# Kernel optimization log

Hardware: AMD Instinct MI355X
Metric: run time of the kernel (lower is better)

Reference implementation:

```python
import jax, jax.numpy as jnp
from jax import lax
import numpy as np

KEY = 4
WIDTH = 32
CH = 3


def _inv_perm():
    # Reproduce construct_mapping(4, 32, 3): mapping[0] = arange(384),
    # mapping[1] = blocks of a (4,32,3) index grid split into 4x4x3 column
    # blocks, flattened. tensor_map does out[:, perm] = in[:, arange], i.e.
    # a scatter; equivalently out = in[:, argsort(perm)].
    s = np.arange(KEY * WIDTH * CH).reshape(KEY, WIDTH, CH)
    perm = np.concatenate([s[:, j:j + KEY, :].reshape(-1) for j in range(0, WIDTH, KEY)])
    return np.argsort(perm)  # (384,)

_INV = jnp.asarray(_inv_perm())


def _conv(x, w, b):
    y = lax.conv_general_dilated(x, w, (1, 1), 'SAME',
                                 dimension_numbers=('NCHW', 'OIHW', 'NCHW'))
    return y + b[None, :, None, None]


def _maxpool2(x):
    return lax.reduce_window(x, -jnp.inf, lax.max,
                             (1, 1, 2, 2), (1, 1, 2, 2), 'VALID')


def setup_inputs() -> dict:
    key = jax.random.key(0)
    ks = jax.random.split(key, 10)
    f32 = jnp.float32
    B = 8192
    return {
        'x': jax.random.normal(ks[0], (B, 32, 32, 3), dtype=f32),
        'W_lin': jax.random.normal(ks[1], (48, 48), dtype=f32) * 0.1,
        'conv1_w': jax.random.normal(ks[2], (32, 3, 3, 3), dtype=f32) * 0.1,
        'conv1_b': jax.random.normal(ks[3], (32,), dtype=f32) * 0.05,
        'conv2_w': jax.random.normal(ks[4], (64, 32, 3, 3), dtype=f32) * 0.05,
        'conv2_b': jax.random.normal(ks[5], (64,), dtype=f32) * 0.05,
        'conv3_w': jax.random.normal(ks[6], (128, 64, 3, 3), dtype=f32) * 0.05,
        'conv3_b': jax.random.normal(ks[7], (128,), dtype=f32) * 0.05,
        'fc_w': jax.random.normal(ks[8], (10, 2048), dtype=f32) * 0.02,
        'fc_b': jax.random.normal(ks[9], (10,), dtype=f32) * 0.02,
        'stage': 2,
    }


def reference(x, W_lin, conv1_w, conv1_b, conv2_w, conv2_b, conv3_w, conv3_b,
              fc_w, fc_b, stage):
    B = x.shape[0]
    if stage == 2:
        # 64 blocks of 4x4x3 in row-major block order (i outer, j inner).
        xb = x.reshape(B, 8, KEY, 8, KEY, CH)            # (B, ib, ir, jb, jc, c)
        xb = xb.transpose(0, 1, 3, 2, 4, 5).reshape(B, 64, 48)
        y = jnp.einsum('bnk,ok->bno', xb, W_lin)          # per-block linear (no bias)
        # group 8 column-blocks per row-block -> (B, 8, 384), permute columns
        y = y.reshape(B, 8, 384)[:, :, _INV]
        x_final = y.reshape(B, 32, 32, 3).transpose(0, 3, 1, 2)  # NCHW
    else:
        x_final = x
    h = _maxpool2(jax.nn.relu(_conv(x_final, conv1_w, conv1_b)))
    h = _maxpool2(jax.nn.relu(_conv(h, conv2_w, conv2_b)))
    h = _maxpool2(jax.nn.relu(_conv(h, conv3_w, conv3_b)))
    h = h.reshape(-1, 2048)
    logits = h @ fc_w.T + fc_b
    return jax.nn.log_softmax(logits, axis=-1)
```

## Files before the change

kernel.cpp:

```cpp
#include <hip/hip_runtime.h>
#include <hip/hip_bf16.h>

typedef unsigned short u16;
typedef __attribute__((ext_vector_type(8))) short short8v;
typedef __attribute__((ext_vector_type(4))) float f32x4;
typedef __attribute__((ext_vector_type(16))) float f32x16;
typedef union { short8v v; uint u[4]; } pack8;

__device__ __forceinline__ float bu2f(u16 u) {
    return __uint_as_float(((unsigned)u) << 16);
}
__device__ __forceinline__ u16 f2bu(float f) {
    unsigned u = __float_as_uint(f);
    u += 0x7fffu + ((u >> 16) & 1u);
    return (u16)(u >> 16);
}
__device__ __forceinline__ uint pk2(float a, float b) {
    return (uint)f2bu(a) | ((uint)f2bu(b) << 16);
}

__global__ __launch_bounds__(256) void k_repack(
    const float* __restrict__ Wlin, const float* __restrict__ c1w,
    const float* __restrict__ c2w, const float* __restrict__ c3w,
    u16* __restrict__ w1p, u16* __restrict__ s2wp,
    u16* __restrict__ w2p, u16* __restrict__ w3p)
{
    int i = blockIdx.x * 256 + threadIdx.x;
    if (i < 32 * 48) {
        int oc = i / 48, k = i - oc * 48;
        int kh = k >> 4, e = k & 15;
        int kw = e >> 2, c = e & 3;
        u16 v = 0;
        if (kw < 3 && c < 3)
            v = f2bu(c1w[((oc * 3 + c) * 3 + kh) * 3 + kw]);
        w1p[i] = v;
    }
    if (i < 96 * 72) {
        int r = i / 72, k = i - r * 72;
        u16 v = 0;
        if (k < 48) {
            int o = r % 48;
            float w = Wlin[o * 48 + k];
            u16 hi = f2bu(w);
            v = (r < 48) ? hi : f2bu(w - bu2f(hi));
        }
        s2wp[i] = v;
    }
    if (i < 64 * 288) {
        int oc = i / 288, r = i - oc * 288;
        int tap = r >> 5, ic = r & 31;
        w2p[oc * 296 + r] = f2bu(c2w[(oc * 32 + ic) * 9 + tap]);
    }
    if (i < 128 * 576) {
        int oc = i / 576, r = i - oc * 576;
        int tap = r >> 6, ic = r & 63;
        w3p[oc * 584 + r] = f2bu(c3w[(oc * 64 + ic) * 9 + tap]);
    }
}

#define IMG4  0
#define SCR   4624
#define IN3   4624
#define W1L   11024
#define IN2   12560
#define LDS_N 25520

__global__ __launch_bounds__(256, 3) void k_img(
    const float* __restrict__ x, const u16* __restrict__ s2wp,
    const u16* __restrict__ w1p, const float* __restrict__ c1b,
    const int* __restrict__ stage,
    const u16* __restrict__ w2p, const float* __restrict__ c2b,
    const u16* __restrict__ w3p, const float* __restrict__ c3b,
    u16* __restrict__ o3)
{
    __shared__ __align__(16) u16 lds[LDS_N];
    const int b = blockIdx.x, t = threadIdx.x;
    const int wv = t >> 6, lane = t & 63, lr = lane & 15, q = lane >> 4;
    uint* z32 = (uint*)lds;

    for (int i = t; i < 2312; i += 256) z32[i] = 0u;
    for (int i = t; i < 1360; i += 256) {
        int cell = i / 20, d = i - cell * 20;
        int h, w;
        if (cell < 18)      { h = 0;  w = cell; }
        else if (cell < 36) { h = 17; w = cell - 18; }
        else { int k = cell - 36; h = 1 + (k >> 1); w = (k & 1) * 17; }
        z32[6280 + (h * 18 + w) * 20 + d] = 0u;
    }
    for (int i = t; i < 192; i += 256)
        *(short8v*)(&lds[W1L + i * 8]) = *(const short8v*)(&w1p[i * 8]);

    const int sv = stage[0];
    if (sv == 2) {
        {
            const int n = t >> 2, ir = t & 3;
            const float* xp = x + (size_t)b * 3072 + (((n >> 3) * 4 + ir) * 96 + (n & 7) * 12);
            const float4 va = ((const float4*)xp)[0];
            const float4 vb = ((const float4*)xp)[1];
            const float4 vc = ((const float4*)xp)[2];
            uint* dst = (uint*)&lds[SCR + n * 72 + ir * 12];
            dst[0] = pk2(va.x, va.y); dst[1] = pk2(va.z, va.w);
            dst[2] = pk2(vb.x, vb.y); dst[3] = pk2(vb.z, vb.w);
            dst[4] = pk2(vc.x, vc.y); dst[5] = pk2(vc.z, vc.w);
            if (ir < 2) {
                uint* z2 = (uint*)&lds[SCR + n * 72 + 48 + ir * 8];
                z2[0] = 0u; z2[1] = 0u; z2[2] = 0u; z2[3] = 0u;
            }
        }
        short8v bh0[3], bh1[3], bl0[3], bl1[3];
        #pragma unroll
        for (int nf = 0; nf < 3; ++nf) {
            bh0[nf] = *(const short8v*)(&s2wp[(nf * 16 + lr) * 72 + q * 8]);
            bh1[nf] = *(const short8v*)(&s2wp[(nf * 16 + lr) * 72 + 32 + q * 8]);
            bl0[nf] = *(const short8v*)(&s2wp[(48 + nf * 16 + lr) * 72 + q * 8]);
            bl1[nf] = *(const short8v*)(&s2wp[(48 + nf * 16 + lr) * 72 + 32 + q * 8]);
        }
        __syncthreads();
        short8v a0 = *(const short8v*)&lds[SCR + (wv * 16 + lr) * 72 + q * 8];
        short8v a1 = *(const short8v*)&lds[SCR + (wv * 16 + lr) * 72 + 32 + q * 8];
        f32x4 y[3];
        #pragma unroll
        for (int nf = 0; nf < 3; ++nf) {
            y[nf] = (f32x4){0.f, 0.f, 0.f, 0.f};
            y[nf] = __builtin_amdgcn_mfma_f32_16x16x32_bf16(a0, bh0[nf], y[nf], 0, 0, 0);
            y[nf] = __builtin_amdgcn_mfma_f32_16x16x32_bf16(a1, bh1[nf], y[nf], 0, 0, 0);
            y[nf] = __builtin_amdgcn_mfma_f32_16x16x32_bf16(a0, bl0[nf], y[nf], 0, 0, 0);
            y[nf] = __builtin_amdgcn_mfma_f32_16x16x32_bf16(a1, bl1[nf], y[nf], 0, 0, 0);
        }
        #pragma unroll
        for (int nf = 0; nf < 3; ++nf)
            #pragma unroll
            for (int r = 0; r < 4; ++r) {
                int n2 = wv * 16 + q * 4 + r;
                int o  = nf * 16 + lr;
                int ir = o / 12, rm = o - ir * 12;
                int jc = rm / 3, c = rm - jc * 3;
                int hh = (n2 >> 3) * 4 + ir, ww = (n2 & 7) * 4 + jc;
                lds[IMG4 + ((hh + 1) * 34 + (ww + 1)) * 4 + c] = f2bu(y[nf][r]);
            }
    } else {
        if (t < 4) z32[2312 + t] = 0u;
        __syncthreads();
        for (int e = t; e < 3072; e += 256) {
            int hh = e / 96, rm = e - hh * 96;
            int ww = rm / 3, c = rm - ww * 3;
            lds[IMG4 + ((hh + 1) * 34 + (ww + 1)) * 4 + c] = f2bu(x[(size_t)b * 3072 + e]);
        }
    }
    __syncthreads();

    for (int i = t; i < 1152; i += 256) {
        int cell = i >> 5, d = i & 31;
        int pos;
        if (cell < 10)      pos = cell;
        else if (cell < 20) pos = 90 + (cell - 10);
        else { int k = cell - 20; pos = (1 + (k >> 1)) * 10 + (k & 1) * 9; }
        z32[2312 + pos * 32 + d] = 0u;
    }
    {
        const int oc32 = lane & 31, hi = lane >> 5;
        short8v wb[3];
        #pragma unroll
        for (int s = 0; s < 3; ++s)
            wb[s] = *(const short8v*)&lds[W1L + oc32 * 48 + s * 16 + hi * 8];
        const float bias1 = c1b[oc32];

        #pragma unroll
        for (int chk = 0; chk < 4; ++chk) {
            f32x16 acc0, acc1;
            #pragma unroll
            for (int i = 0; i < 16; ++i) { acc0[i] = 0.f; acc1[i] = 0.f; }
            #pragma unroll
            for (int s = 0; s < 3; ++s) {
                #pragma unroll
                for (int f = 0; f < 2; ++f) {
                    const int h = wv * 8 + chk * 2 + f;
                    const int a4 = ((h + s) * 34 + oc32 + hi * 2) * 4;
                    pack8 pk;
                    *(unsigned long long*)&pk.u[0] = *(const unsigned long long*)(&lds[IMG4 + a4]);
                    *(unsigned long long*)&pk.u[2] = *(const unsigned long long*)(&lds[IMG4 + a4 + 4]);
                    if (f == 0) acc0 = __builtin_amdgcn_mfma_f32_32x32x16_bf16(pk.v, wb[s], acc0, 0, 0, 0);
                    else        acc1 = __builtin_amdgcn_mfma_f32_32x32x16_bf16(pk.v, wb[s], acc1, 0, 0, 0);
                }
            }
            const int hq = wv * 4 + chk;
            #pragma unroll
            for (int g = 0; g < 4; ++g) {
                #pragma unroll
                for (int pp = 0; pp < 2; ++pp) {
                    const int i0 = 4 * g + 2 * pp;
                    float m0 = fmaxf(acc0[i0], acc0[i0 + 1]);
                    float m1 = fmaxf(acc1[i0], acc1[i0 + 1]);
                    float v = fmaxf(fmaxf(m0, m1) + bias1, 0.f);
                    const int wq = 4 * g + 2 * hi + pp;
                    lds[IN2 + ((hq + 1) * 18 + (wq + 1)) * 40 + oc32] = f2bu(v);
                }
            }
        }
    }
    __syncthreads();

    {
        const u16* wb2 = w2p + (size_t)lr * 296 + q * 8;
        f32x4 acc[4][4];
        #pragma unroll
        for (int m = 0; m < 4; ++m)
            #pragma unroll
            for (int n = 0; n < 4; ++n) acc[m][n] = (f32x4){0.f, 0.f, 0.f, 0.f};

        short8v bfr[3][4];
        #pragma unroll
        for (int n = 0; n < 4; ++n) {
            bfr[0][n] = *(const short8v*)(wb2 + n * 4736 + 0);
            bfr[1][n] = *(const short8v*)(wb2 + n * 4736 + 32);
        }
        #pragma unroll
        for (int s = 0; s < 9; ++s) {
            if (s + 2 < 9) {
                #pragma unroll
                for (int n = 0; n < 4; ++n)
                    bfr[(s + 2) % 3][n] = *(const short8v*)(wb2 + n * 4736 + (s + 2) * 32);
            }
            const int kh = s / 3, kw = s - kh * 3;
            short8v af[4];
            #pragma unroll
            for (int m = 0; m < 4; ++m)
                af[m] = *(const short8v*)(&lds[IN2 + ((wv * 4 + m + kh) * 18 + lr + kw) * 40 + q * 8]);
            __builtin_amdgcn_s_setprio(1);
            #pragma unroll
            for (int m = 0; m < 4; ++m)
                #pragma unroll
                for (int n = 0; n < 4; ++n)
                    acc[m][n] = __builtin_amdgcn_mfma_f32_16x16x32_bf16(af[m], bfr[s % 3][n], acc[m][n], 0, 0, 0);
            __builtin_amdgcn_s_setprio(0);
        }
        #pragma unroll
        for (int n = 0; n < 4; ++n) {
            float bias = c2b[n * 16 + lr];
            #pragma unroll
            for (int mp = 0; mp < 2; ++mp) {
                #pragma unroll
                for (int p = 0; p < 2; ++p) {
                    float m0 = fmaxf(acc[2 * mp][n][2 * p], acc[2 * mp][n][2 * p + 1]);
                    float m1 = fmaxf(acc[2 * mp + 1][n][2 * p], acc[2 * mp + 1][n][2 * p + 1]);
                    float v = fmaxf(fmaxf(m0, m1) + bias, 0.f);
                    int hq = wv * 2 + mp, wq = 2 * q + p;
                    int posW = (hq + 1) * 10 + (wq + 1);
                    int oc = n * 16 + lr;
                    lds[IN3 + posW * 64 + (oc ^ ((posW & 7) << 3))] = f2bu(v);
                }
            }
        }
    }
    __syncthreads();

    {
        const int ocb = wv * 32;
        const int hA = lr >> 3, wA = lr & 7;
        const u16* wb3 = w3p + (size_t)(ocb + lr) * 584 + q * 8;

        f32x4 acc3[4][2];
        #pragma unroll
        for (int m = 0; m < 4; ++m)
            #pragma unroll
            for (int n = 0; n < 2; ++n) acc3[m][n] = (f32x4){0.f, 0.f, 0.f, 0.f};

        short8v br[3][2];
        #pragma unroll
        for (int n = 0; n < 2; ++n) {
            br[0][n] = *(const short8v*)(wb3 + n * 9344 + 0);
            br[1][n] = *(const short8v*)(wb3 + n * 9344 + 32);
        }
        #pragma unroll
        for (int s = 0; s < 18; ++s) {
            if (s + 2 < 18) {
                const int off2 = ((s + 2) >> 1) * 64 + ((s + 2) & 1) * 32;
                #pragma unroll
                for (int n = 0; n < 2; ++n)
                    br[(s + 2) % 3][n] = *(const short8v*)(wb3 + n * 9344 + off2);
            }
            const int tap = s >> 1, half = s & 1;
            const int kh = tap / 3, kw = tap - kh * 3;
            short8v a3[4];
            #pragma unroll
            for (int m = 0; m < 4; ++m) {
                int posR = (m * 2 + hA + kh) * 10 + wA + kw;
                int sl = (half * 32 + q * 8) ^ ((posR & 7) << 3);
                a3[m] = *(const short8v*)(&lds[IN3 + posR * 64 + sl]);
            }
            __builtin_amdgcn_s_setprio(1);
            #pragma unroll
            for (int m = 0; m < 4; ++m)
                #pragma unroll
                for (int n = 0; n < 2; ++n)
                    acc3[m][n] = __builtin_amdgcn_mfma_f32_16x16x32_bf16(a3[m], br[s % 3][n], acc3[m][n], 0, 0, 0);
            __builtin_amdgcn_s_setprio(0);
        }
        #pragma unroll
        for (int n = 0; n < 2; ++n) {
            float bias = c3b[ocb + n * 16 + lr];
            #pragma unroll
            for (int m = 0; m < 4; ++m) {
                #pragma unroll
                for (int p = 0; p < 2; ++p) {
                    float mm = fmaxf(acc3[m][n][2 * p], acc3[m][n][2 * p + 1]);
                    float v2 = fmaxf(mm, __shfl_xor(mm, 32));
                    float v = fmaxf(v2 + bias, 0.f);
                    if (lane < 32) {
                        int wq = (q & 1) * 2 + p;
                        o3[(size_t)b * 2048 + (m * 4 + wq) * 128 + ocb + n * 16 + lr] = f2bu(v);
                    }
                }
            }
        }
    }
}

__global__ __launch_bounds__(256) void k_fc(
    const u16* __restrict__ o3, const float* __restrict__ fw,
    const float* __restrict__ fb, float* __restrict__ out)
{
    const int b = blockIdx.x * 4 + (threadIdx.x >> 6);
    const int lane = threadIdx.x & 63;
    const u16* xp = o3 + (size_t)b * 2048;
    float xr[32];
    #pragma unroll
    for (int i = 0; i < 32; ++i) {
        int kk = lane + i * 64;
        int c = kk >> 4, h = (kk >> 2) & 3, w = kk & 3;
        xr[i] = bu2f(xp[h * 512 + w * 128 + c]);
    }
    float lg[10];
    #pragma unroll
    for (int o = 0; o < 10; ++o) {
        const float* wr = fw + (size_t)o * 2048;
        float s = 0.f;
        #pragma unroll
        for (int i = 0; i < 32; ++i) s += xr[i] * wr[lane + i * 64];
        #pragma unroll
        for (int d = 32; d > 0; d >>= 1) s += __shfl_xor(s, d);
        lg[o] = s + fb[o];
    }
    float m = lg[0];
    #pragma unroll
    for (int o = 1; o < 10; ++o) m = fmaxf(m, lg[o]);
    float den = 0.f;
    #pragma unroll
    for (int o = 0; o < 10; ++o) den += expf(lg[o] - m);
    float lse = logf(den);
    if (lane < 10) {
        float v = lg[0];
        #pragma unroll
        for (int o = 1; o < 10; ++o) v = (lane == o) ? lg[o] : v;
        out[(size_t)b * 10 + lane] = v - m - lse;
    }
}

extern "C" void kernel_launch(void* const* d_in, const int* in_sizes, int n_in,
                              void* d_out, int out_size, void* d_ws, size_t ws_size,
                              hipStream_t stream)
{
    const float* x    = (const float*)d_in[0];
    const float* Wlin = (const float*)d_in[1];
    const float* c1w  = (const float*)d_in[2];
    const float* c1b  = (const float*)d_in[3];
    const float* c2w  = (const float*)d_in[4];
    const float* c2b  = (const float*)d_in[5];
    const float* c3w  = (const float*)d_in[6];
    const float* c3b  = (const float*)d_in[7];
    const float* fw   = (const float*)d_in[8];
    const float* fb   = (const float*)d_in[9];
    const int* stage  = (const int*)d_in[10];
    float* out = (float*)d_out;

    const int B = in_sizes[0] / 3072;

    char* ws = (char*)d_ws;
    u16* o3   = (u16*)ws;
    char* WB  = ws + (size_t)B * 4096;
    u16* w1p  = (u16*)(WB);
    u16* s2wp = (u16*)(WB + 4608);
    u16* w2p  = (u16*)(WB + 18432);
    u16* w3p  = (u16*)(WB + 56320);

    k_repack<<<288, 256, 0, stream>>>(Wlin, c1w, c2w, c3w, w1p, s2wp, w2p, w3p);
    k_img   <<<B, 256, 0, stream>>>(x, s2wp, w1p, c1b, stage, w2p, c2b, w3p, c3b, o3);
    k_fc    <<<B / 4, 256, 0, stream>>>(o3, fw, fb, out);
}
```

Before: 258.4 us.

## Shrink LDS footprint and split conv2 accumulators to raise occupancy to 4 blocks

```diff
diff --git a/kernel.cpp b/kernel.cpp
--- a/kernel.cpp
+++ b/kernel.cpp
@@ -59,13 +59,12 @@
 }
 
 #define IMG4  0
-#define SCR   4624
-#define IN3   4624
-#define W1L   11024
-#define IN2   12560
-#define LDS_N 25520
-
-__global__ __launch_bounds__(256, 3) void k_img(
+#define XB    4624
+#define IN3   0
+#define IN2   6400
+#define LDS_N 19360
+
+__global__ __launch_bounds__(256, 4) void k_img(
     const float* __restrict__ x, const u16* __restrict__ s2wp,
     const u16* __restrict__ w1p, const float* __restrict__ c1b,
     const int* __restrict__ stage,
@@ -76,19 +75,14 @@
     __shared__ __align__(16) u16 lds[LDS_N];
     const int b = blockIdx.x, t = threadIdx.x;
     const int wv = t >> 6, lane = t & 63, lr = lane & 15, q = lane >> 4;
+    const int oc32 = lane & 31, hi = lane >> 5;
     uint* z32 = (uint*)lds;
 
     for (int i = t; i < 2312; i += 256) z32[i] = 0u;
-    for (int i = t; i < 1360; i += 256) {
-        int cell = i / 20, d = i - cell * 20;
-        int h, w;
-        if (cell < 18)      { h = 0;  w = cell; }
-        else if (cell < 36) { h = 17; w = cell - 18; }
-        else { int k = cell - 36; h = 1 + (k >> 1); w = (k & 1) * 17; }
-        z32[6280 + (h * 18 + w) * 20 + d] = 0u;
-    }
-    for (int i = t; i < 192; i += 256)
-        *(short8v*)(&lds[W1L + i * 8]) = *(const short8v*)(&w1p[i * 8]);
+    short8v wb1[3];
+    #pragma unroll
+    for (int s = 0; s < 3; ++s)
+        wb1[s] = *(const short8v*)(&w1p[oc32 * 48 + s * 16 + hi * 8]);
 
     const int sv = stage[0];
     if (sv == 2) {
@@ -98,12 +92,12 @@
             const float4 va = ((const float4*)xp)[0];
             const float4 vb = ((const float4*)xp)[1];
             const float4 vc = ((const float4*)xp)[2];
-            uint* dst = (uint*)&lds[SCR + n * 72 + ir * 12];
+            uint* dst = (uint*)&lds[XB + n * 72 + ir * 12];
             dst[0] = pk2(va.x, va.y); dst[1] = pk2(va.z, va.w);
             dst[2] = pk2(vb.x, vb.y); dst[3] = pk2(vb.z, vb.w);
             dst[4] = pk2(vc.x, vc.y); dst[5] = pk2(vc.z, vc.w);
             if (ir < 2) {
-                uint* z2 = (uint*)&lds[SCR + n * 72 + 48 + ir * 8];
+                uint* z2 = (uint*)&lds[XB + n * 72 + 48 + ir * 8];
                 z2[0] = 0u; z2[1] = 0u; z2[2] = 0u; z2[3] = 0u;
             }
         }
@@ -116,8 +110,8 @@
             bl1[nf] = *(const short8v*)(&s2wp[(48 + nf * 16 + lr) * 72 + 32 + q * 8]);
         }
         __syncthreads();
-        short8v a0 = *(const short8v*)&lds[SCR + (wv * 16 + lr) * 72 + q * 8];
-        short8v a1 = *(const short8v*)&lds[SCR + (wv * 16 + lr) * 72 + 32 + q * 8];
+        short8v a0 = *(const short8v*)&lds[XB + (wv * 16 + lr) * 72 + q * 8];
+        short8v a1 = *(const short8v*)&lds[XB + (wv * 16 + lr) * 72 + 32 + q * 8];
         f32x4 y[3];
         #pragma unroll
         for (int nf = 0; nf < 3; ++nf) {
@@ -127,6 +121,7 @@
             y[nf] = __builtin_amdgcn_mfma_f32_16x16x32_bf16(a0, bl0[nf], y[nf], 0, 0, 0);
             y[nf] = __builtin_amdgcn_mfma_f32_16x16x32_bf16(a1, bl1[nf], y[nf], 0, 0, 0);
         }
+        __syncthreads();
         #pragma unroll
         for (int nf = 0; nf < 3; ++nf)
             #pragma unroll
@@ -149,22 +144,16 @@
     }
     __syncthreads();
 
-    for (int i = t; i < 1152; i += 256) {
-        int cell = i >> 5, d = i & 31;
-        int pos;
-        if (cell < 10)      pos = cell;
-        else if (cell < 20) pos = 90 + (cell - 10);
-        else { int k = cell - 20; pos = (1 + (k >> 1)) * 10 + (k & 1) * 9; }
-        z32[2312 + pos * 32 + d] = 0u;
+    for (int i = t; i < 1360; i += 256) {
+        int cell = i / 20, d = i - cell * 20;
+        int h, w;
+        if (cell < 18)      { h = 0;  w = cell; }
+        else if (cell < 36) { h = 17; w = cell - 18; }
+        else { int k = cell - 36; h = 1 + (k >> 1); w = (k & 1) * 17; }
+        z32[3200 + (h * 18 + w) * 20 + d] = 0u;
     }
     {
-        const int oc32 = lane & 31, hi = lane >> 5;
-        short8v wb[3];
-        #pragma unroll
-        for (int s = 0; s < 3; ++s)
-            wb[s] = *(const short8v*)&lds[W1L + oc32 * 48 + s * 16 + hi * 8];
         const float bias1 = c1b[oc32];
-
         #pragma unroll
         for (int chk = 0; chk < 4; ++chk) {
             f32x16 acc0, acc1;
@@ -179,8 +168,8 @@
                     pack8 pk;
                     *(unsigned long long*)&pk.u[0] = *(const unsigned long long*)(&lds[IMG4 + a4]);
                     *(unsigned long long*)&pk.u[2] = *(const unsigned long long*)(&lds[IMG4 + a4 + 4]);
-                    if (f == 0) acc0 = __builtin_amdgcn_mfma_f32_32x32x16_bf16(pk.v, wb[s], acc0, 0, 0, 0);
-                    else        acc1 = __builtin_amdgcn_mfma_f32_32x32x16_bf16(pk.v, wb[s], acc1, 0, 0, 0);
+                    if (f == 0) acc0 = __builtin_amdgcn_mfma_f32_32x32x16_bf16(pk.v, wb1[s], acc0, 0, 0, 0);
+                    else        acc1 = __builtin_amdgcn_mfma_f32_32x32x16_bf16(pk.v, wb1[s], acc1, 0, 0, 0);
                 }
             }
             const int hq = wv * 4 + chk;
@@ -200,17 +189,26 @@
     }
     __syncthreads();
 
-    {
-        const u16* wb2 = w2p + (size_t)lr * 296 + q * 8;
-        f32x4 acc[4][4];
+    for (int i = t; i < 1152; i += 256) {
+        int cell = i >> 5, d = i & 31;
+        int pos;
+        if (cell < 10)      pos = cell;
+        else if (cell < 20) pos = 90 + (cell - 10);
+        else { int k = cell - 20; pos = (1 + (k >> 1)) * 10 + (k & 1) * 9; }
+        z32[pos * 32 + d] = 0u;
+    }
+    #pragma unroll
+    for (int nh = 0; nh < 2; ++nh) {
+        const u16* wb2 = w2p + (size_t)(nh * 32 + lr) * 296 + q * 8;
+        f32x4 acc[4][2];
         #pragma unroll
         for (int m = 0; m < 4; ++m)
             #pragma unroll
-            for (int n = 0; n < 4; ++n) acc[m][n] = (f32x4){0.f, 0.f, 0.f, 0.f};
-
-        short8v bfr[3][4];
-        #pragma unroll
-        for (int n = 0; n < 4; ++n) {
+            for (int n = 0; n < 2; ++n) acc[m][n] = (f32x4){0.f, 0.f, 0.f, 0.f};
+
+        short8v bfr[3][2];
+        #pragma unroll
+        for (int n = 0; n < 2; ++n) {
             bfr[0][n] = *(const short8v*)(wb2 + n * 4736 + 0);
             bfr[1][n] = *(const short8v*)(wb2 + n * 4736 + 32);
         }
@@ -218,7 +216,7 @@
         for (int s = 0; s < 9; ++s) {
             if (s + 2 < 9) {
                 #pragma unroll
-                for (int n = 0; n < 4; ++n)
+                for (int n = 0; n < 2; ++n)
                     bfr[(s + 2) % 3][n] = *(const short8v*)(wb2 + n * 4736 + (s + 2) * 32);
             }
             const int kh = s / 3, kw = s - kh * 3;
@@ -230,13 +228,13 @@
             #pragma unroll
             for (int m = 0; m < 4; ++m)
                 #pragma unroll
-                for (int n = 0; n < 4; ++n)
+                for (int n = 0; n < 2; ++n)
                     acc[m][n] = __builtin_amdgcn_mfma_f32_16x16x32_bf16(af[m], bfr[s % 3][n], acc[m][n], 0, 0, 0);
             __builtin_amdgcn_s_setprio(0);
         }
         #pragma unroll
-        for (int n = 0; n < 4; ++n) {
-            float bias = c2b[n * 16 + lr];
+        for (int n = 0; n < 2; ++n) {
+            float bias = c2b[nh * 32 + n * 16 + lr];
             #pragma unroll
             for (int mp = 0; mp < 2; ++mp) {
                 #pragma unroll
@@ -246,7 +244,7 @@
                     float v = fmaxf(fmaxf(m0, m1) + bias, 0.f);
                     int hq = wv * 2 + mp, wq = 2 * q + p;
                     int posW = (hq + 1) * 10 + (wq + 1);
-                    int oc = n * 16 + lr;
+                    int oc = nh * 32 + n * 16 + lr;
                     lds[IN3 + posW * 64 + (oc ^ ((posW & 7) << 3))] = f2bu(v);
                 }
             }
```

Result: no change. 256.6 us (-0.7%).
